# Kernel optimization log

Hardware: AMD Instinct MI355X
Metric: run time of the kernel (lower is better)

The kernel has to match this reference:

```python
import jax, jax.numpy as jnp
import numpy as np

B, S, D_IN, D_OUT = 4, 2048, 4096, 16384


def setup_inputs() -> dict:
    key = jax.random.key(0)
    k1, k2, k3, k4 = jax.random.split(key, 4)
    x = jax.random.normal(k1, (B, S, D_IN), dtype=jnp.float32)
    # per-channel symmetric int8 weights, [out_features, in_features]
    weight_int8 = jax.random.randint(k2, (D_OUT, D_IN), -128, 128, dtype=jnp.int32).astype(jnp.int8)
    # per-channel weight scales (positive, realistic magnitude)
    weight_scale = jax.random.uniform(k3, (D_OUT,), dtype=jnp.float32) * 0.01 + 1e-4
    # static per-tensor activation scale (calibrated constant)
    act_scale = jnp.float32(0.02)
    bias = jax.random.normal(k4, (D_OUT,), dtype=jnp.float32) * 0.1
    return {"x": x, "weight_int8": weight_int8, "weight_scale": weight_scale,
            "act_scale": act_scale, "bias": bias}


def reference(x, weight_int8, weight_scale, act_scale, bias):
    orig_shape = x.shape
    orig_dtype = x.dtype
    x2d = x.reshape(-1, orig_shape[-1])  # [M, D_in]
    # static per-tensor symmetric activation quantization
    x_int8 = jnp.clip(jnp.round(x2d.astype(jnp.float32) / act_scale), -128, 127).astype(jnp.int8)
    y_int32 = jnp.matmul(x_int8, weight_int8.T, preferred_element_type=jnp.int32)  # [M, D_out]
    output_scale = (act_scale * weight_scale).astype(jnp.float32)  # [D_out]
    y = y_int32.astype(jnp.float32) * output_scale[None, :] + bias.astype(jnp.float32)[None, :]
    return y.reshape(*orig_shape[:-1], y.shape[-1]).astype(orig_dtype)
```

## Files before the change

### kernel.cpp

```cpp
#include <hip/hip_runtime.h>
#include <stdint.h>

#define GAS __attribute__((address_space(1)))
#define LAS __attribute__((address_space(3)))

typedef int v4i __attribute__((ext_vector_type(4)));

constexpr int Mdim = 8192;
constexpr int Ndim = 16384;
constexpr int Kdim = 4096;

__device__ __forceinline__ int pack4i8(int a, int b, int c, int d) {
    return (a & 255) | ((b & 255) << 8) | ((c & 255) << 16) | ((d & 255) << 24);
}

__device__ __forceinline__ int qz(float v, float inv) {
    return (int)fminf(fmaxf(rintf(v * inv), -128.0f), 127.0f);
}

__global__ void k_quant_x(const float* __restrict__ x, const float* __restrict__ asc,
                          int8_t* __restrict__ xq) {
    const int i = blockIdx.x * blockDim.x + threadIdx.x;
    const float inv = 1.0f / *asc;
    const float4* xv = (const float4*)x + (size_t)i * 4;
    float4 f0 = xv[0], f1 = xv[1], f2 = xv[2], f3 = xv[3];
    int4 o;
    o.x = pack4i8(qz(f0.x, inv), qz(f0.y, inv), qz(f0.z, inv), qz(f0.w, inv));
    o.y = pack4i8(qz(f1.x, inv), qz(f1.y, inv), qz(f1.z, inv), qz(f1.w, inv));
    o.z = pack4i8(qz(f2.x, inv), qz(f2.y, inv), qz(f2.z, inv), qz(f2.w, inv));
    o.w = pack4i8(qz(f3.x, inv), qz(f3.y, inv), qz(f3.z, inv), qz(f3.w, inv));
    ((int4*)xq)[i] = o;
}

__global__ void k_pack_w(const int* __restrict__ w, int8_t* __restrict__ wp) {
    const int c = blockIdx.x * blockDim.x + threadIdx.x;
    const int l = c & 63, ks = (c >> 6) & 63, nt = c >> 12;
    const int n = nt * 16 + (l & 15);
    const int k = (ks << 6) + ((l >> 4) << 4);
    const int4* src = (const int4*)(w + (size_t)n * Kdim + k);
    int4 a = src[0], b = src[1], cc = src[2], d = src[3];
    int4 o;
    o.x = pack4i8(a.x, a.y, a.z, a.w);
    o.y = pack4i8(b.x, b.y, b.z, b.w);
    o.z = pack4i8(cc.x, cc.y, cc.z, cc.w);
    o.w = pack4i8(d.x, d.y, d.z, d.w);
    ((int4*)wp)[c] = o;
}

#define VMW(N) asm volatile("s_waitcnt vmcnt(" #N ")" ::: "memory")

#define STEP(T, BC, BN, LB, SA, VMN)                                         \
  {                                                                          \
    VMW(VMN);                                                                \
    __builtin_amdgcn_s_barrier();                                            \
    __builtin_amdgcn_sched_barrier(0);                                       \
    if (LB) {                                                                \
      _Pragma("unroll") for (int f = 0; f < 4; ++f)                          \
        BN[f] = *(const v4i*)(Bp + ((((size_t)(ntb + f)) << 6 | ((T) + 1))   \
                                    << 10) + (lane << 4));                   \
    }                                                                        \
    if (SA) stA((T) + 2);                                                    \
    {                                                                        \
      const int8_t* S_ = lds + (((T) & 3) << 14);                            \
      v4i a_[8];                                                             \
      _Pragma("unroll") for (int f = 0; f < 8; ++f)                          \
        a_[f] = *(const v4i*)(S_ + aoff + f * 1024);                         \
      __builtin_amdgcn_s_setprio(1);                                         \
      _Pragma("unroll") for (int fi = 0; fi < 8; ++fi)                       \
        _Pragma("unroll") for (int fj = 0; fj < 4; ++fj)                     \
          acc[fi][fj] = __builtin_amdgcn_mfma_i32_16x16x64_i8(               \
              a_[fi], BC[fj], acc[fi][fj], 0, 0, 0);                         \
      __builtin_amdgcn_s_setprio(0);                                         \
    }                                                                        \
  }

__global__ __launch_bounds__(256, 2)
void k_gemm_bp(const int8_t* __restrict__ Aq, const int8_t* __restrict__ Bp,
               const float* __restrict__ wscale, const float* __restrict__ asc,
               const float* __restrict__ bias, float* __restrict__ out) {
    __shared__ __align__(16) int8_t lds[65536];
    const int tid = threadIdx.x, lane = tid & 63, w = tid >> 6;
    const int wm = w >> 1, wn = w & 1;
    const int lrow = lane & 15, kgrp = lane >> 4;

    const int bid = blockIdx.x;
    const int swz = ((bid & 7) << 9) | (bid >> 3);
    const int mt = swz & 31, nt = swz >> 5;
    const int m0 = mt << 8, n0 = nt << 7;

    const int srow = tid >> 2;
    const int scol = (((tid & 3) ^ ((tid >> 3) & 3)) << 4);
    const int8_t* gA[4];
#pragma unroll
    for (int u = 0; u < 4; ++u)
        gA[u] = Aq + (size_t)(m0 + u * 64 + srow) * Kdim + scol;
    const int dstoff = w << 10;

    auto stA = [&](int t) {
        int8_t* base = lds + ((t & 3) << 14) + dstoff;
        const int kb = t << 6;
#pragma unroll
        for (int u = 0; u < 4; ++u)
            __builtin_amdgcn_global_load_lds((const GAS void*)(gA[u] + kb),
                                             (LAS void*)(base + u * 4096), 16, 0, 0);
    };

    const int ntb = (n0 >> 4) + (wn << 2);

    const int kc = (kgrp ^ ((lrow >> 1) & 3)) << 4;
    const int aoff = ((wm << 7) + lrow) * 64 + kc;

    v4i acc[8][4];
#pragma unroll
    for (int i = 0; i < 8; ++i)
#pragma unroll
        for (int j = 0; j < 4; ++j) acc[i][j] = (v4i){0, 0, 0, 0};

    v4i bP[4], bQ[4];

    stA(0); stA(1);
#pragma unroll
    for (int f = 0; f < 4; ++f)
        bP[f] = *(const v4i*)(Bp + ((((size_t)(ntb + f)) << 6) << 10) + (lane << 4));

    for (int j = 0; j < 15; ++j) {
        const int t = j << 2;
        STEP(t + 0, bP, bQ, 1, 1, 8)
        STEP(t + 1, bQ, bP, 1, 1, 8)
        STEP(t + 2, bP, bQ, 1, 1, 8)
        STEP(t + 3, bQ, bP, 1, 1, 8)
    }
    STEP(60, bP, bQ, 1, 1, 8)
    STEP(61, bQ, bP, 1, 1, 8)
    STEP(62, bP, bQ, 1, 0, 8)
    STEP(63, bQ, bP, 0, 0, 4)

    const float ascale = *asc;
#pragma unroll
    for (int fj = 0; fj < 4; ++fj) {
        const int col = n0 + (wn << 6) + fj * 16 + lrow;
        const float sc = ascale * wscale[col];
        const float bb = bias[col];
#pragma unroll
        for (int mi = 0; mi < 8; ++mi) {
            const int r0 = m0 + (wm << 7) + mi * 16 + (kgrp << 2);
            float* o = out + (size_t)r0 * Ndim + col;
#pragma unroll
            for (int q = 0; q < 4; ++q)
                o[(size_t)q * Ndim] = (float)acc[mi][fj][q] * sc + bb;
        }
    }
}

template <bool AQ>
__global__ __launch_bounds__(256)
void k_gemm(const int8_t* __restrict__ Aq, const float* __restrict__ Xf,
            const int* __restrict__ W32,
            const float* __restrict__ wscale, const float* __restrict__ asc,
            const float* __restrict__ bias, float* __restrict__ out) {
    constexpr int BM = 128, BN = 128, BK = 64;
    constexpr int KT = Kdim / BK;
    __shared__ __align__(16) int8_t As[2][BM * BK];
    __shared__ __align__(16) int8_t Bs[2][BN * BK];

    const int tid  = threadIdx.x;
    const int lane = tid & 63;
    const int wid  = tid >> 6;
    const int wm = wid >> 1, wn = wid & 1;
    const int lrow = lane & 15, kgrp = lane >> 4;

    const int cpx = gridDim.x >> 3;
    const int swz = ((int)blockIdx.x & 7) * cpx + ((int)blockIdx.x >> 3);
    const int mt = swz & (Mdim / BM - 1);
    const int nt = swz / (Mdim / BM);
    const int m0 = mt * BM, n0 = nt * BN;

    const float ascale = *asc;
    const float inv = 1.0f / ascale;

    v4i acc[4][4];
#pragma unroll
    for (int i = 0; i < 4; ++i)
#pragma unroll
        for (int j = 0; j < 4; ++j) acc[i][j] = (v4i){0, 0, 0, 0};

    auto stage = [&](int buf, int kt) {
        const int k0 = kt * BK;
        if constexpr (AQ) {
            int8_t* ldsp = &As[buf][wid << 10];
            const int8_t* g = Aq + (size_t)(m0 + (tid >> 2)) * Kdim + k0 + ((tid & 3) << 4);
            __builtin_amdgcn_global_load_lds((const GAS void*)g, (LAS void*)ldsp, 16, 0, 0);
            __builtin_amdgcn_global_load_lds((const GAS void*)(g + (size_t)64 * Kdim),
                                             (LAS void*)(ldsp + 4096), 16, 0, 0);
        } else {
            const int row = tid >> 1, cb = (tid & 1) << 5;
            const float4* src = (const float4*)(Xf + (size_t)(m0 + row) * Kdim + k0 + cb);
            int t[8];
#pragma unroll
            for (int j = 0; j < 8; ++j) {
                float4 f = src[j];
                t[j] = pack4i8(qz(f.x, inv), qz(f.y, inv), qz(f.z, inv), qz(f.w, inv));
            }
            int4* dst = (int4*)&As[buf][row * BK + cb];
            dst[0] = make_int4(t[0], t[1], t[2], t[3]);
            dst[1] = make_int4(t[4], t[5], t[6], t[7]);
        }
        {
            const int row = tid >> 1, cb = (tid & 1) << 5;
            const int4* src = (const int4*)(W32 + (size_t)(n0 + row) * Kdim + k0 + cb);
            int t[8];
#pragma unroll
            for (int j = 0; j < 8; ++j) {
                int4 vv = src[j];
                t[j] = pack4i8(vv.x, vv.y, vv.z, vv.w);
            }
            int4* dst = (int4*)&Bs[buf][row * BK + cb];
            dst[0] = make_int4(t[0], t[1], t[2], t[3]);
            dst[1] = make_int4(t[4], t[5], t[6], t[7]);
        }
    };

    stage(0, 0);
    for (int kt = 0; kt < KT; ++kt) {
        const int cur = kt & 1;
        __syncthreads();
        if (kt + 1 < KT) stage(cur ^ 1, kt + 1);

        v4i a[4], b[4];
        const int koff = kgrp << 4;
#pragma unroll
        for (int i = 0; i < 4; ++i) {
            a[i] = *(const v4i*)&As[cur][(wm * 64 + i * 16 + lrow) * BK + koff];
            b[i] = *(const v4i*)&Bs[cur][(wn * 64 + i * 16 + lrow) * BK + koff];
        }
#pragma unroll
        for (int i = 0; i < 4; ++i)
#pragma unroll
            for (int j = 0; j < 4; ++j)
                acc[i][j] = __builtin_amdgcn_mfma_i32_16x16x64_i8(a[i], b[j], acc[i][j], 0, 0, 0);
    }

#pragma unroll
    for (int j = 0; j < 4; ++j) {
        const int col = n0 + wn * 64 + j * 16 + lrow;
        const float sc = ascale * wscale[col];
        const float bb = bias[col];
#pragma unroll
        for (int i = 0; i < 4; ++i) {
            const int r0 = m0 + wm * 64 + i * 16 + (kgrp << 2);
            float* o = out + (size_t)r0 * Ndim + col;
#pragma unroll
            for (int r = 0; r < 4; ++r)
                o[(size_t)r * Ndim] = (float)acc[i][j][r] * sc + bb;
        }
    }
}

extern "C" void kernel_launch(void* const* d_in, const int* in_sizes, int n_in,
                              void* d_out, int out_size, void* d_ws, size_t ws_size,
                              hipStream_t stream) {
    const float* x      = (const float*)d_in[0];
    const int*   w32    = (const int*)d_in[1];
    const float* wscale = (const float*)d_in[2];
    const float* asc    = (const float*)d_in[3];
    const float* bias   = (const float*)d_in[4];
    float* out = (float*)d_out;

    const size_t nx = (size_t)Mdim * Kdim;
    const size_t nw = (size_t)Ndim * Kdim;
    int8_t* xq = (int8_t*)d_ws;
    int8_t* wp = xq + nx;

    const bool haveX = ws_size >= nx;
    const bool haveW = ws_size >= nx + nw;

    if (haveX) k_quant_x<<<(int)(nx / 16 / 256), 256, 0, stream>>>(x, asc, xq);
    if (haveW) k_pack_w<<<(int)(nw / 16 / 256), 256, 0, stream>>>(w32, wp);

    if (haveW) {
        dim3 grid((Mdim / 256) * (Ndim / 128));
        k_gemm_bp<<<grid, 256, 0, stream>>>(xq, wp, wscale, asc, bias, out);
    } else if (haveX) {
        dim3 grid((Mdim / 128) * (Ndim / 128));
        k_gemm<true><<<grid, 256, 0, stream>>>(xq, x, w32, wscale, asc, bias, out);
    } else {
        dim3 grid((Mdim / 128) * (Ndim / 128));
        k_gemm<false><<<grid, 256, 0, stream>>>(xq, x, w32, wscale, asc, bias, out);
    }
}
```

Baseline: 962.8 us.

## Enlarge GEMM tile to 256x256 with 512 threads and superstage LDS double-buffering

Replaces the 256x128 block GEMM with a 256x256 tile run by 8 waves, which halves A-tile reloads per output column. A now streams into a 128KB LDS split into two 4-k-step superstages, so the kernel hits a barrier once every four k-steps instead of every step. Each wave still computes a 128x64 sub-tile and keeps its per-lane B fragment register double-buffering. The 128KB LDS per block with 512 threads risks limiting occupancy to one block per CU even though launch bounds request two, and the coarser sync makes latency hiding depend on prefetching a full superstage ahead.

```diff
diff --git a/kernel.cpp b/kernel.cpp
--- a/kernel.cpp
+++ b/kernel.cpp
@@ -47,68 +47,64 @@
     ((int4*)wp)[c] = o;
 }
 
-#define VMW(N) asm volatile("s_waitcnt vmcnt(" #N ")" ::: "memory")
-
-#define STEP(T, BC, BN, LB, SA, VMN)                                         \
-  {                                                                          \
-    VMW(VMN);                                                                \
-    __builtin_amdgcn_s_barrier();                                            \
-    __builtin_amdgcn_sched_barrier(0);                                       \
-    if (LB) {                                                                \
-      _Pragma("unroll") for (int f = 0; f < 4; ++f)                          \
-        BN[f] = *(const v4i*)(Bp + ((((size_t)(ntb + f)) << 6 | ((T) + 1))   \
-                                    << 10) + (lane << 4));                   \
-    }                                                                        \
-    if (SA) stA((T) + 2);                                                    \
-    {                                                                        \
-      const int8_t* S_ = lds + (((T) & 3) << 14);                            \
-      v4i a_[8];                                                             \
-      _Pragma("unroll") for (int f = 0; f < 8; ++f)                          \
-        a_[f] = *(const v4i*)(S_ + aoff + f * 1024);                         \
-      __builtin_amdgcn_s_setprio(1);                                         \
-      _Pragma("unroll") for (int fi = 0; fi < 8; ++fi)                       \
-        _Pragma("unroll") for (int fj = 0; fj < 4; ++fj)                     \
-          acc[fi][fj] = __builtin_amdgcn_mfma_i32_16x16x64_i8(               \
-              a_[fi], BC[fj], acc[fi][fj], 0, 0, 0);                         \
-      __builtin_amdgcn_s_setprio(0);                                         \
-    }                                                                        \
+
+#define KSTEP(BUF, KSL, T, BCUR, BNXT, ST, LB)                                 \
+  {                                                                            \
+    v4i afr[8];                                                                \
+    _Pragma("unroll") for (int f = 0; f < 8; ++f)                              \
+      afr[f] = *(const v4i*)(lds + (BUF) * 65536 + (KSL) * 16384 + arow + f * 1024); \
+    if (ST) {                                                                  \
+      int8_t* d = lds + ((BUF) ^ 1) * 65536 + (KSL) * 16384 + dstoff;          \
+      const int8_t* s = rowA0 + ((T) + 4) * 64;                                \
+      __builtin_amdgcn_global_load_lds((const GAS void*)s, (LAS void*)d, 16, 0, 0); \
+      __builtin_amdgcn_global_load_lds((const GAS void*)(s + rb1off),          \
+                                       (LAS void*)(d + 8192), 16, 0, 0);       \
+    }                                                                          \
+    if (LB) {                                                                  \
+      _Pragma("unroll") for (int f = 0; f < 4; ++f)                            \
+        BNXT[f] = *(const v4i*)(pB[f] + (((T) + 1) << 10));                    \
+    }                                                                          \
+    __builtin_amdgcn_s_setprio(1);                                             \
+    _Pragma("unroll") for (int fi = 0; fi < 8; ++fi)                           \
+      _Pragma("unroll") for (int fj = 0; fj < 4; ++fj)                         \
+        acc[fi][fj] = __builtin_amdgcn_mfma_i32_16x16x64_i8(                   \
+            afr[fi], BCUR[fj], acc[fi][fj], 0, 0, 0);                          \
+    __builtin_amdgcn_s_setprio(0);                                             \
   }
 
-__global__ __launch_bounds__(256, 2)
-void k_gemm_bp(const int8_t* __restrict__ Aq, const int8_t* __restrict__ Bp,
+#define SS_BARRIER                                                             \
+  asm volatile("s_waitcnt vmcnt(0)" ::: "memory");                             \
+  __builtin_amdgcn_s_barrier();                                                \
+  __builtin_amdgcn_sched_barrier(0);
+
+__global__ __launch_bounds__(512, 2)
+void k_gemm_ss(const int8_t* __restrict__ Aq, const int8_t* __restrict__ Bp,
                const float* __restrict__ wscale, const float* __restrict__ asc,
                const float* __restrict__ bias, float* __restrict__ out) {
-    __shared__ __align__(16) int8_t lds[65536];
+    __shared__ __align__(16) int8_t lds[131072];
     const int tid = threadIdx.x, lane = tid & 63, w = tid >> 6;
-    const int wm = w >> 1, wn = w & 1;
+    const int wm = w >> 2, wn = w & 3;
     const int lrow = lane & 15, kgrp = lane >> 4;
 
     const int bid = blockIdx.x;
-    const int swz = ((bid & 7) << 9) | (bid >> 3);
+    const int swz = ((bid & 7) << 8) | (bid >> 3);
     const int mt = swz & 31, nt = swz >> 5;
-    const int m0 = mt << 8, n0 = nt << 7;
+    const int m0 = mt << 8, n0 = nt << 8;
 
     const int srow = tid >> 2;
     const int scol = (((tid & 3) ^ ((tid >> 3) & 3)) << 4);
-    const int8_t* gA[4];
-#pragma unroll
-    for (int u = 0; u < 4; ++u)
-        gA[u] = Aq + (size_t)(m0 + u * 64 + srow) * Kdim + scol;
+    const int8_t* rowA0 = Aq + (size_t)(m0 + srow) * Kdim + scol;
+    const size_t rb1off = (size_t)128 * Kdim;
     const int dstoff = w << 10;
 
-    auto stA = [&](int t) {
-        int8_t* base = lds + ((t & 3) << 14) + dstoff;
-        const int kb = t << 6;
-#pragma unroll
-        for (int u = 0; u < 4; ++u)
-            __builtin_amdgcn_global_load_lds((const GAS void*)(gA[u] + kb),
-                                             (LAS void*)(base + u * 4096), 16, 0, 0);
-    };
-
     const int ntb = (n0 >> 4) + (wn << 2);
+    const int8_t* pB[4];
+#pragma unroll
+    for (int f = 0; f < 4; ++f)
+        pB[f] = Bp + (((size_t)(ntb + f)) << 16) + (lane << 4);
 
     const int kc = (kgrp ^ ((lrow >> 1) & 3)) << 4;
-    const int aoff = ((wm << 7) + lrow) * 64 + kc;
+    const int arow = ((wm << 7) + lrow) * 64 + kc;
 
     v4i acc[8][4];
 #pragma unroll
@@ -118,22 +114,40 @@
 
     v4i bP[4], bQ[4];
 
-    stA(0); stA(1);
-#pragma unroll
-    for (int f = 0; f < 4; ++f)
-        bP[f] = *(const v4i*)(Bp + ((((size_t)(ntb + f)) << 6) << 10) + (lane << 4));
-
-    for (int j = 0; j < 15; ++j) {
-        const int t = j << 2;
-        STEP(t + 0, bP, bQ, 1, 1, 8)
-        STEP(t + 1, bQ, bP, 1, 1, 8)
-        STEP(t + 2, bP, bQ, 1, 1, 8)
-        STEP(t + 3, bQ, bP, 1, 1, 8)
-    }
-    STEP(60, bP, bQ, 1, 1, 8)
-    STEP(61, bQ, bP, 1, 1, 8)
-    STEP(62, bP, bQ, 1, 0, 8)
-    STEP(63, bQ, bP, 0, 0, 4)
+#pragma unroll
+    for (int ks = 0; ks < 4; ++ks) {
+        int8_t* d = lds + ks * 16384 + dstoff;
+        const int8_t* s = rowA0 + ks * 64;
+        __builtin_amdgcn_global_load_lds((const GAS void*)s, (LAS void*)d, 16, 0, 0);
+        __builtin_amdgcn_global_load_lds((const GAS void*)(s + rb1off),
+                                         (LAS void*)(d + 8192), 16, 0, 0);
+    }
+#pragma unroll
+    for (int f = 0; f < 4; ++f) bP[f] = *(const v4i*)(pB[f]);
+    SS_BARRIER
+
+    for (int p = 0; p < 7; ++p) {
+        const int t0 = p << 3;
+        KSTEP(0, 0, t0 + 0, bP, bQ, 1, 1)
+        KSTEP(0, 1, t0 + 1, bQ, bP, 1, 1)
+        KSTEP(0, 2, t0 + 2, bP, bQ, 1, 1)
+        KSTEP(0, 3, t0 + 3, bQ, bP, 1, 1)
+        SS_BARRIER
+        KSTEP(1, 0, t0 + 4, bP, bQ, 1, 1)
+        KSTEP(1, 1, t0 + 5, bQ, bP, 1, 1)
+        KSTEP(1, 2, t0 + 6, bP, bQ, 1, 1)
+        KSTEP(1, 3, t0 + 7, bQ, bP, 1, 1)
+        SS_BARRIER
+    }
+    KSTEP(0, 0, 56, bP, bQ, 1, 1)
+    KSTEP(0, 1, 57, bQ, bP, 1, 1)
+    KSTEP(0, 2, 58, bP, bQ, 1, 1)
+    KSTEP(0, 3, 59, bQ, bP, 1, 1)
+    SS_BARRIER
+    KSTEP(1, 0, 60, bP, bQ, 0, 1)
+    KSTEP(1, 1, 61, bQ, bP, 0, 1)
+    KSTEP(1, 2, 62, bP, bQ, 0, 1)
+    KSTEP(1, 3, 63, bQ, bP, 0, 0)
 
     const float ascale = *asc;
 #pragma unroll
@@ -278,8 +292,8 @@
     if (haveW) k_pack_w<<<(int)(nw / 16 / 256), 256, 0, stream>>>(w32, wp);
 
     if (haveW) {
-        dim3 grid((Mdim / 256) * (Ndim / 128));
-        k_gemm_bp<<<grid, 256, 0, stream>>>(xq, wp, wscale, asc, bias, out);
+        dim3 grid((Mdim / 256) * (Ndim / 256));
+        k_gemm_ss<<<grid, 512, 0, stream>>>(xq, wp, wscale, asc, bias, out);
     } else if (haveX) {
         dim3 grid((Mdim / 128) * (Ndim / 128));
         k_gemm<true><<<grid, 256, 0, stream>>>(xq, x, w32, wscale, asc, bias, out);
```

Result: faster. 869.9 us (-9.7%).
